# Optimization experiments

Measured on AMD Instinct MI355X. Metric: run time of the kernel, lower is better.

## Reference

```python
import jax, jax.numpy as jnp
import numpy as np

D_MODEL = 768
N_HEADS = 12
HEAD_DIM = D_MODEL // N_HEADS
D_FF = 4 * D_MODEL
EPS = 1e-5


def setup_inputs() -> dict:
    key = jax.random.key(0)
    ks = jax.random.split(key, 16)
    s = 0.02
    x = jax.random.normal(ks[0], (2, 2048, D_MODEL), dtype=jnp.float32)
    wq = jax.random.normal(ks[1], (D_MODEL, D_MODEL), dtype=jnp.float32) * s
    bq = jnp.zeros((D_MODEL,), jnp.float32)
    wk = jax.random.normal(ks[2], (D_MODEL, D_MODEL), dtype=jnp.float32) * s
    bk = jnp.zeros((D_MODEL,), jnp.float32)
    wv = jax.random.normal(ks[3], (D_MODEL, D_MODEL), dtype=jnp.float32) * s
    bv = jnp.zeros((D_MODEL,), jnp.float32)
    wo = jax.random.normal(ks[4], (D_MODEL, D_MODEL), dtype=jnp.float32) * s
    bo = jnp.zeros((D_MODEL,), jnp.float32)
    w1 = jax.random.normal(ks[5], (D_MODEL, D_FF), dtype=jnp.float32) * s
    b1 = jnp.zeros((D_FF,), jnp.float32)
    w2 = jax.random.normal(ks[6], (D_FF, D_MODEL), dtype=jnp.float32) * s
    b2 = jnp.zeros((D_MODEL,), jnp.float32)
    ln1_g = jnp.ones((D_MODEL,), jnp.float32)
    ln1_b = jnp.zeros((D_MODEL,), jnp.float32)
    ln2_g = jnp.ones((D_MODEL,), jnp.float32)
    ln2_b = jnp.zeros((D_MODEL,), jnp.float32)
    return dict(x=x, wq=wq, bq=bq, wk=wk, bk=bk, wv=wv, bv=bv, wo=wo, bo=bo,
                w1=w1, b1=b1, w2=w2, b2=b2,
                ln1_g=ln1_g, ln1_b=ln1_b, ln2_g=ln2_g, ln2_b=ln2_b)


def _layernorm(x, g, b):
    mu = jnp.mean(x, axis=-1, keepdims=True)
    var = jnp.mean(jnp.square(x - mu), axis=-1, keepdims=True)
    return (x - mu) * jax.lax.rsqrt(var + EPS) * g + b


def _attention(x, wq, bq, wk, bk, wv, bv, wo, bo):
    B, S, D = x.shape
    def split_heads(t):  # [B,S,D] -> [B,H,S,Hd]
        return t.reshape(B, S, N_HEADS, HEAD_DIM).transpose(0, 2, 1, 3)
    q = split_heads(x @ wq + bq)
    k = split_heads(x @ wk + bk)
    v = split_heads(x @ wv + bv)
    scores = jnp.einsum('bhqd,bhkd->bhqk', q, k) / np.sqrt(HEAD_DIM).astype(np.float32)
    causal = jnp.tril(jnp.ones((S, S), dtype=bool))
    scores = jnp.where(causal, scores, -jnp.inf)
    weights = jax.nn.softmax(scores, axis=-1)
    attn = jnp.einsum('bhqk,bhkd->bhqd', weights, v)
    attn = attn.transpose(0, 2, 1, 3).reshape(B, S, D)
    return attn @ wo + bo


def reference(x, wq, bq, wk, bk, wv, bv, wo, bo, w1, b1, w2, b2,
              ln1_g, ln1_b, ln2_g, ln2_b):
    x = x + _attention(_layernorm(x, ln1_g, ln1_b), wq, bq, wk, bk, wv, bv, wo, bo)
    h = _layernorm(x, ln2_g, ln2_b)
    ff = jax.nn.relu(h @ w1 + b1) @ w2 + b2
    return x + ff
```

## Files before the change

kernel.cpp:

```cpp
#include <hip/hip_runtime.h>
#include <stdint.h>

typedef __bf16 bf16;
typedef float f32x4 __attribute__((ext_vector_type(4)));
typedef bf16 bf16x8 __attribute__((ext_vector_type(8)));
typedef bf16 bf16x4 __attribute__((ext_vector_type(4)));

#define MFMA16(a, b, c) __builtin_amdgcn_mfma_f32_16x16x32_bf16((a), (b), (c), 0, 0, 0)

static __device__ __forceinline__ void load_lds16(const bf16* g, bf16* l) {
  __builtin_amdgcn_global_load_lds(
      (const __attribute__((address_space(1))) void*)g,
      (__attribute__((address_space(3))) void*)l, 16, 0, 0);
}

__global__ void __launch_bounds__(256) k_transpose(
    const float* s0, const float* s1, const float* s2, const float* s3,
    const float* s4, const float* s5,
    bf16* d0, bf16* d1, bf16* d2, bf16* d3, bf16* d4, bf16* d5) {
  int z = blockIdx.z;
  const float* src; bf16* dst; int R, C;
  switch (z) {
    case 0: src = s0; dst = d0; R = 768;  C = 768;  break;
    case 1: src = s1; dst = d1; R = 768;  C = 768;  break;
    case 2: src = s2; dst = d2; R = 768;  C = 768;  break;
    case 3: src = s3; dst = d3; R = 768;  C = 768;  break;
    case 4: src = s4; dst = d4; R = 768;  C = 3072; break;
    default: src = s5; dst = d5; R = 3072; C = 768; break;
  }
  int tcn = C >> 5;
  int nt = (R >> 5) * tcn;
  int t = blockIdx.x;
  if (t >= nt) return;
  int tr = t / tcn, tc = t % tcn;
  __shared__ float tile[32][33];
  int tx = threadIdx.x & 31, ty = threadIdx.x >> 5;
  for (int i = 0; i < 4; i++)
    tile[ty + i * 8][tx] = src[(size_t)(tr * 32 + ty + i * 8) * C + tc * 32 + tx];
  __syncthreads();
  for (int i = 0; i < 4; i++)
    dst[(size_t)(tc * 32 + ty + i * 8) * R + tr * 32 + tx] = (bf16)tile[tx][ty + i * 8];
}

__global__ void __launch_bounds__(256) k_layernorm(
    const float* __restrict__ in, const float* __restrict__ gam,
    const float* __restrict__ bet, bf16* __restrict__ out) {
  int row = blockIdx.x, tid = threadIdx.x;
  const float* rp = in + (size_t)row * 768;
  float v0 = rp[tid], v1 = rp[tid + 256], v2 = rp[tid + 512];
  float s = v0 + v1 + v2, sq = v0 * v0 + v1 * v1 + v2 * v2;
  for (int off = 1; off < 64; off <<= 1) {
    s += __shfl_xor(s, off, 64);
    sq += __shfl_xor(sq, off, 64);
  }
  __shared__ float ps[8];
  if ((tid & 63) == 0) { ps[tid >> 6] = s; ps[4 + (tid >> 6)] = sq; }
  __syncthreads();
  s = ps[0] + ps[1] + ps[2] + ps[3];
  sq = ps[4] + ps[5] + ps[6] + ps[7];
  float mu = s * (1.0f / 768.0f);
  float rstd = rsqrtf(sq * (1.0f / 768.0f) - mu * mu + 1e-5f);
  bf16* op = out + (size_t)row * 768;
  op[tid] = (bf16)((v0 - mu) * rstd * gam[tid] + bet[tid]);
  op[tid + 256] = (bf16)((v1 - mu) * rstd * gam[tid + 256] + bet[tid + 256]);
  op[tid + 512] = (bf16)((v2 - mu) * rstd * gam[tid + 512] + bet[tid + 512]);
}

__global__ void __launch_bounds__(256) k_ln2_reduce(
    const float* __restrict__ p0, const float* __restrict__ p1,
    const float* __restrict__ x, const float* __restrict__ bo,
    const float* __restrict__ gam, const float* __restrict__ bet,
    float* __restrict__ x1, bf16* __restrict__ h2) {
  int row = blockIdx.x, tid = threadIdx.x;
  size_t base = (size_t)row * 768;
  float v0 = p0[base + tid] + p1[base + tid] + x[base + tid] + bo[tid];
  float v1 = p0[base + tid + 256] + p1[base + tid + 256] + x[base + tid + 256] + bo[tid + 256];
  float v2 = p0[base + tid + 512] + p1[base + tid + 512] + x[base + tid + 512] + bo[tid + 512];
  x1[base + tid] = v0; x1[base + tid + 256] = v1; x1[base + tid + 512] = v2;
  float s = v0 + v1 + v2, sq = v0 * v0 + v1 * v1 + v2 * v2;
  for (int off = 1; off < 64; off <<= 1) {
    s += __shfl_xor(s, off, 64);
    sq += __shfl_xor(sq, off, 64);
  }
  __shared__ float ps[8];
  if ((tid & 63) == 0) { ps[tid >> 6] = s; ps[4 + (tid >> 6)] = sq; }
  __syncthreads();
  s = ps[0] + ps[1] + ps[2] + ps[3];
  sq = ps[4] + ps[5] + ps[6] + ps[7];
  float mu = s * (1.0f / 768.0f);
  float rstd = rsqrtf(sq * (1.0f / 768.0f) - mu * mu + 1e-5f);
  bf16* op = h2 + base;
  op[tid] = (bf16)((v0 - mu) * rstd * gam[tid] + bet[tid]);
  op[tid + 256] = (bf16)((v1 - mu) * rstd * gam[tid + 256] + bet[tid + 256]);
  op[tid + 512] = (bf16)((v2 - mu) * rstd * gam[tid + 512] + bet[tid + 512]);
}

__global__ void __launch_bounds__(256) k_ff2_reduce(
    const float* __restrict__ f0, const float* __restrict__ f1,
    const float* __restrict__ f2, const float* __restrict__ f3,
    const float* __restrict__ x1, const float* __restrict__ b2,
    float* __restrict__ out) {
  size_t i = ((size_t)blockIdx.x * 256 + threadIdx.x) * 4;
  int col = (int)(i % 768);
  f32x4 v = *(const f32x4*)(x1 + i);
  f32x4 b = *(const f32x4*)(b2 + col);
  f32x4 a0 = *(const f32x4*)(f0 + i), a1 = *(const f32x4*)(f1 + i);
  f32x4 a2 = *(const f32x4*)(f2 + i), a3 = *(const f32x4*)(f3 + i);
  *(f32x4*)(out + i) = v + b + a0 + a1 + a2 + a3;
}

template <int MT>
static __device__ __forceinline__ void gemm_core(
    const bf16* __restrict__ A, int lda, const bf16* __restrict__ Bt, int ldb,
    int Kc, int m0, int n0, bf16* As, bf16* Bs, f32x4 acc[MT][4]) {
  int tid = threadIdx.x, w = tid >> 6, lane = tid & 63, quad = lane >> 4, l15 = lane & 15;
  int wr = w >> 1, wc = w & 1;
  int srow = lane >> 2, sk = (lane & 3) * 8;
  const int ABUF = MT * 32 * 32;
  const int BBUF = 128 * 32;

  auto stage = [&](int k0, int buf) {
    bf16* Ab = As + buf * ABUF;
    bf16* Bb = Bs + buf * BBUF;
    if (MT == 4) {
      for (int c = 0; c < 2; c++) {
        int seg = w * 2 + c;
        load_lds16(A + (size_t)(m0 + seg * 16 + srow) * lda + k0 + sk, Ab + seg * 512);
      }
    } else {
      load_lds16(A + (size_t)(m0 + w * 16 + srow) * lda + k0 + sk, Ab + w * 512);
    }
    for (int c = 0; c < 2; c++) {
      int seg = w * 2 + c;
      load_lds16(Bt + (size_t)(n0 + seg * 16 + srow) * ldb + k0 + sk, Bb + seg * 512);
    }
  };

  stage(0, 0);
  int cur = 0;
  for (int k0 = 0; k0 < Kc; k0 += 32) {
    __syncthreads();
    if (k0 + 32 < Kc) stage(k0 + 32, cur ^ 1);
    const bf16* Ab = As + cur * ABUF;
    const bf16* Bb = Bs + cur * BBUF;
    bf16x8 af[MT], bfr[4];
    for (int mi = 0; mi < MT; mi++)
      af[mi] = *(const bf16x8*)(Ab + (wr * (MT * 16) + mi * 16 + l15) * 32 + quad * 8);
    for (int ni = 0; ni < 4; ni++)
      bfr[ni] = *(const bf16x8*)(Bb + (wc * 64 + ni * 16 + l15) * 32 + quad * 8);
    for (int mi = 0; mi < MT; mi++)
      for (int ni = 0; ni < 4; ni++)
        acc[mi][ni] = MFMA16(af[mi], bfr[ni], acc[mi][ni]);
    cur ^= 1;
  }
}

template <int MT>
__global__ void __launch_bounds__(256, 3) k_gemm(
    const bf16* __restrict__ A, const bf16* __restrict__ Bt,
    const float* __restrict__ bias, bf16* __restrict__ outp, int K_, int N_) {
  __shared__ __align__(16) bf16 As[2 * MT * 32 * 32];
  __shared__ __align__(16) bf16 Bs[2 * 128 * 32];
  int m0 = blockIdx.y * (MT * 32), n0 = blockIdx.x * 128;
  f32x4 acc[MT][4] = {};
  gemm_core<MT>(A, K_, Bt, K_, K_, m0, n0, As, Bs, acc);
  int tid = threadIdx.x, w = tid >> 6, lane = tid & 63, quad = lane >> 4, l15 = lane & 15;
  int wr = w >> 1, wc = w & 1;
  float bv[4];
  for (int ni = 0; ni < 4; ni++) bv[ni] = bias[n0 + wc * 64 + ni * 16 + l15];
  for (int mi = 0; mi < MT; mi++) {
    int mb = m0 + wr * (MT * 16) + mi * 16 + quad * 4;
    for (int ni = 0; ni < 4; ni++) {
      int n = n0 + wc * 64 + ni * 16 + l15;
      for (int r = 0; r < 4; r++) {
        float val = acc[mi][ni][r] + bv[ni];
        outp[(size_t)(mb + r) * N_ + n] = (bf16)fmaxf(val, 0.0f);
      }
    }
  }
}

template <int MT>
__global__ void __launch_bounds__(256, 3) k_gemm_split(
    const bf16* __restrict__ A, const bf16* __restrict__ Bt,
    float* __restrict__ f0, float* __restrict__ f1,
    float* __restrict__ f2, float* __restrict__ f3, int K_, int Kc, int N_) {
  __shared__ __align__(16) bf16 As[2 * MT * 32 * 32];
  __shared__ __align__(16) bf16 Bs[2 * 128 * 32];
  int z = blockIdx.z;
  float* outp = (z == 0) ? f0 : (z == 1) ? f1 : (z == 2) ? f2 : f3;
  int m0 = blockIdx.y * (MT * 32), n0 = blockIdx.x * 128;
  f32x4 acc[MT][4] = {};
  gemm_core<MT>(A + (size_t)z * Kc, K_, Bt + (size_t)z * Kc, K_, Kc, m0, n0, As, Bs, acc);
  int tid = threadIdx.x, w = tid >> 6, lane = tid & 63, quad = lane >> 4, l15 = lane & 15;
  int wr = w >> 1, wc = w & 1;
  for (int mi = 0; mi < MT; mi++) {
    int mb = m0 + wr * (MT * 16) + mi * 16 + quad * 4;
    for (int ni = 0; ni < 4; ni++) {
      int n = n0 + wc * 64 + ni * 16 + l15;
      for (int r = 0; r < 4; r++)
        outp[(size_t)(mb + r) * N_ + n] = acc[mi][ni][r];
    }
  }
}

template <int MT>
__global__ void __launch_bounds__(256, 3) k_gemm_qkv(
    const bf16* __restrict__ h1, const bf16* __restrict__ wqT,
    const bf16* __restrict__ wkT, const bf16* __restrict__ wvT,
    const float* __restrict__ bq, const float* __restrict__ bk,
    const float* __restrict__ bv, bf16* __restrict__ qb,
    bf16* __restrict__ kb, bf16* __restrict__ vtb) {
  __shared__ __align__(16) bf16 As[2 * MT * 32 * 32];
  __shared__ __align__(16) bf16 Bs[2 * 128 * 32];
  int z = blockIdx.z;
  const bf16* Bt = (z == 0) ? wqT : (z == 1) ? wkT : wvT;
  const float* bias = (z == 0) ? bq : (z == 1) ? bk : bv;
  int m0 = blockIdx.y * (MT * 32), n0 = blockIdx.x * 128;
  f32x4 acc[MT][4] = {};
  gemm_core<MT>(h1, 768, Bt, 768, 768, m0, n0, As, Bs, acc);
  int tid = threadIdx.x, w = tid >> 6, lane = tid & 63, quad = lane >> 4, l15 = lane & 15;
  int wr = w >> 1, wc = w & 1;
  float bvv[4];
  for (int ni = 0; ni < 4; ni++) bvv[ni] = bias[n0 + wc * 64 + ni * 16 + l15];
  for (int mi = 0; mi < MT; mi++) {
    int mb = m0 + wr * (MT * 16) + mi * 16 + quad * 4;
    int b = mb >> 11, s0_ = mb & 2047;
    for (int ni = 0; ni < 4; ni++) {
      int n = n0 + wc * 64 + ni * 16 + l15;
      int h = n >> 6, hd = n & 63;
      if (z < 2) {
        bf16* outp = (z == 0) ? qb : kb;
        size_t base = (size_t)(b * 12 + h) * 2048 * 64;
        for (int r = 0; r < 4; r++)
          outp[base + (size_t)(s0_ + r) * 64 + hd] = (bf16)(acc[mi][ni][r] + bvv[ni]);
      } else {
        bf16x4 pk;
        for (int r = 0; r < 4; r++) pk[r] = (bf16)(acc[mi][ni][r] + bvv[ni]);
        *(bf16x4*)(vtb + (((size_t)(b * 12 + h) * 64 + hd) * 2048 + s0_)) = pk;
      }
    }
  }
}

__global__ void __launch_bounds__(256, 3) k_attn(
    const bf16* __restrict__ qb, const bf16* __restrict__ kb,
    const bf16* __restrict__ vtb, bf16* __restrict__ out) {
  __shared__ __align__(16) bf16 Ks[2 * 128 * 64];
  __shared__ __align__(16) bf16 Ps[4][16 * 128];
  int qt = 31 - (blockIdx.x / 24);
  int bh = blockIdx.x % 24;
  int q0 = qt * 64;
  int tid = threadIdx.x, w = tid >> 6, lane = tid & 63, quad = lane >> 4, l15 = lane & 15;
  const bf16* qbase = qb + (size_t)bh * 2048 * 64;
  const bf16* kbase = kb + (size_t)bh * 2048 * 64;
  const bf16* vbase = vtb + (size_t)bh * 64 * 2048;

  bf16x8 qf[2];
  for (int ds = 0; ds < 2; ds++)
    qf[ds] = *(const bf16x8*)(qbase + (size_t)(q0 + w * 16 + l15) * 64 + ds * 32 + quad * 8);

  f32x4 o[4] = {};
  f32x4 l_i = {};

  auto stageK = [&](int k0, int buf) {
    int rsub = lane >> 3, c8 = lane & 7;
    bf16* Kb = Ks + buf * (128 * 64);
    for (int c = 0; c < 4; c++) {
      int seg = c * 4 + w;
      int row = seg * 8 + rsub;
      load_lds16(kbase + (size_t)(k0 + row) * 64 + ((c8 ^ (row & 7)) * 8), Kb + seg * 512);
    }
  };

  const float C2 = 0.18033688011112042f;
  int nkt = (qt >> 1) + 1;
  stageK(0, 0);
  int cur = 0;
  for (int kt = 0; kt < nkt; kt++) {
    int k0 = kt * 128;
    __syncthreads();
    if (kt + 1 < nkt) stageK(k0 + 128, cur ^ 1);
    const bf16* Kb = Ks + cur * (128 * 64);

    f32x4 sc[8] = {};
    for (int kj = 0; kj < 8; kj++) {
      int krow = kj * 16 + l15;
      for (int ds = 0; ds < 2; ds++) {
        bf16x8 kf = *(const bf16x8*)(Kb + krow * 64 + (((ds * 4 + quad) ^ (krow & 7)) * 8));
        sc[kj] = MFMA16(qf[ds], kf, sc[kj]);
      }
    }
    if (kt == nkt - 1) {
      int qg = q0 + w * 16 + quad * 4;
      for (int kj = 0; kj < 8; kj++) {
        int kg = k0 + kj * 16 + l15;
        for (int r = 0; r < 4; r++)
          if (kg > qg + r) sc[kj][r] = -3.0e38f;
      }
    }
    f32x4 lsum = {};
    for (int kj = 0; kj < 8; kj++)
      for (int r = 0; r < 4; r++) {
        float p = exp2f(sc[kj][r] * C2);
        sc[kj][r] = p;
        lsum[r] += p;
      }
    for (int off = 1; off < 16; off <<= 1)
      for (int r = 0; r < 4; r++) lsum[r] += __shfl_xor(lsum[r], off, 64);
    for (int r = 0; r < 4; r++) l_i[r] += lsum[r];
    for (int kj = 0; kj < 8; kj++) {
      int colb = kj * 16 + l15;
      int chb = colb >> 3, cin = colb & 7;
      for (int r = 0; r < 4; r++) {
        int prow = quad * 4 + r;
        Ps[w][prow * 128 + ((chb ^ prow) * 8) + cin] = (bf16)sc[kj][r];
      }
    }
    for (int ks = 0; ks < 4; ks++) {
      int prow = l15;
      bf16x8 pf = *(const bf16x8*)(&Ps[w][prow * 128 + (((ks * 4 + quad) ^ prow) * 8)]);
      for (int dj = 0; dj < 4; dj++) {
        int vrow = dj * 16 + l15;
        bf16x8 vf = *(const bf16x8*)(vbase + (size_t)vrow * 2048 + k0 + (ks * 4 + quad) * 8);
        o[dj] = MFMA16(pf, vf, o[dj]);
      }
    }
    cur ^= 1;
  }
  int b = bh / 12, h = bh % 12;
  f32x4 rl;
  for (int r = 0; r < 4; r++) rl[r] = 1.0f / l_i[r];
  int srow = q0 + w * 16 + quad * 4;
  for (int dj = 0; dj < 4; dj++) {
    int d = h * 64 + dj * 16 + l15;
    for (int r = 0; r < 4; r++)
      out[(size_t)(b * 2048 + srow + r) * 768 + d] = (bf16)(o[dj][r] * rl[r]);
  }
}

extern "C" void kernel_launch(void* const* d_in, const int* in_sizes, int n_in,
                              void* d_out, int out_size, void* d_ws, size_t ws_size,
                              hipStream_t stream) {
  const float* x    = (const float*)d_in[0];
  const float* wq   = (const float*)d_in[1];
  const float* bq   = (const float*)d_in[2];
  const float* wk   = (const float*)d_in[3];
  const float* bk   = (const float*)d_in[4];
  const float* wv   = (const float*)d_in[5];
  const float* bv   = (const float*)d_in[6];
  const float* wo   = (const float*)d_in[7];
  const float* bo   = (const float*)d_in[8];
  const float* w1   = (const float*)d_in[9];
  const float* b1   = (const float*)d_in[10];
  const float* w2   = (const float*)d_in[11];
  const float* b2   = (const float*)d_in[12];
  const float* ln1g = (const float*)d_in[13];
  const float* ln1b = (const float*)d_in[14];
  const float* ln2g = (const float*)d_in[15];
  const float* ln2b = (const float*)d_in[16];

  char* p = (char*)d_ws;
  bf16* wqT = (bf16*)p; p += (size_t)768 * 768 * 2;
  bf16* wkT = (bf16*)p; p += (size_t)768 * 768 * 2;
  bf16* wvT = (bf16*)p; p += (size_t)768 * 768 * 2;
  bf16* woT = (bf16*)p; p += (size_t)768 * 768 * 2;
  bf16* w1T = (bf16*)p; p += (size_t)768 * 3072 * 2;
  bf16* w2T = (bf16*)p; p += (size_t)768 * 3072 * 2;
  bf16* h1   = (bf16*)p; p += (size_t)4096 * 768 * 2;
  bf16* qbuf = (bf16*)p; p += (size_t)4096 * 768 * 2;
  bf16* kbuf = (bf16*)p; p += (size_t)4096 * 768 * 2;
  bf16* vtb  = (bf16*)p; p += (size_t)4096 * 768 * 2;
  bf16* att  = (bf16*)p; p += (size_t)4096 * 768 * 2;
  float* x1  = (float*)p; p += (size_t)4096 * 768 * 4;
  bf16* h2   = (bf16*)p; p += (size_t)4096 * 768 * 2;
  bf16* ffm  = (bf16*)p; p += (size_t)4096 * 3072 * 2;
  float* p0  = (float*)p; p += (size_t)4096 * 768 * 4;
  float* p1  = (float*)p; p += (size_t)4096 * 768 * 4;
  float* f0 = (float*)h1;
  float* f1 = (float*)kbuf;
  float* f2 = p0;
  float* f3 = p1;

  k_transpose<<<dim3(2304, 1, 6), dim3(256), 0, stream>>>(
      wq, wk, wv, wo, w1, w2, wqT, wkT, wvT, woT, w1T, w2T);
  k_layernorm<<<dim3(4096), dim3(256), 0, stream>>>(x, ln1g, ln1b, h1);
  k_gemm_qkv<2><<<dim3(6, 64, 3), dim3(256), 0, stream>>>(
      h1, wqT, wkT, wvT, bq, bk, bv, qbuf, kbuf, vtb);
  k_attn<<<dim3(768), dim3(256), 0, stream>>>(qbuf, kbuf, vtb, att);
  k_gemm_split<2><<<dim3(6, 64, 2), dim3(256), 0, stream>>>(
      att, woT, p0, p1, p0, p1, 768, 384, 768);
  k_ln2_reduce<<<dim3(4096), dim3(256), 0, stream>>>(
      p0, p1, x, bo, ln2g, ln2b, x1, h2);
  k_gemm<4><<<dim3(24, 32), dim3(256), 0, stream>>>(
      h2, w1T, b1, ffm, 768, 3072);
  k_gemm_split<4><<<dim3(6, 32, 4), dim3(256), 0, stream>>>(
      ffm, w2T, f0, f1, f2, f3, 3072, 768, 768);
  k_ff2_reduce<<<dim3(3072), dim3(256), 0, stream>>>(
      f0, f1, f2, f3, x1, b2, (float*)d_out);
}
```

Measured before the change: 328.3 us.

## Fuse weight transpose with LN1, stage V tiles in LDS, interleave attention tiles

Merges the weight-transpose and first layernorm kernels into one launch and drops the 6-slice grid that left many blocks idle. In attention, V tiles are now loaded into LDS asynchronously with a swizzled layout instead of read straight from global memory. P is written into the current K buffer after an extra barrier, which frees the separate P array. Query tiles are scheduled alternately from heavy and light causal rows to balance work across blocks. The cost is an extra block-wide sync per key tile and V loads that are not double buffered.

```diff
diff --git a/kernel.cpp b/kernel.cpp
--- a/kernel.cpp
+++ b/kernel.cpp
@@ -14,56 +14,56 @@
       (__attribute__((address_space(3))) void*)l, 16, 0, 0);
 }
 
-__global__ void __launch_bounds__(256) k_transpose(
+__global__ void __launch_bounds__(256) k_prep(
+    const float* __restrict__ x, const float* __restrict__ ln1g,
+    const float* __restrict__ ln1b, bf16* __restrict__ h1,
     const float* s0, const float* s1, const float* s2, const float* s3,
     const float* s4, const float* s5,
     bf16* d0, bf16* d1, bf16* d2, bf16* d3, bf16* d4, bf16* d5) {
-  int z = blockIdx.z;
-  const float* src; bf16* dst; int R, C;
-  switch (z) {
-    case 0: src = s0; dst = d0; R = 768;  C = 768;  break;
-    case 1: src = s1; dst = d1; R = 768;  C = 768;  break;
-    case 2: src = s2; dst = d2; R = 768;  C = 768;  break;
-    case 3: src = s3; dst = d3; R = 768;  C = 768;  break;
-    case 4: src = s4; dst = d4; R = 768;  C = 3072; break;
-    default: src = s5; dst = d5; R = 3072; C = 768; break;
-  }
-  int tcn = C >> 5;
-  int nt = (R >> 5) * tcn;
   int t = blockIdx.x;
-  if (t >= nt) return;
-  int tr = t / tcn, tc = t % tcn;
-  __shared__ float tile[32][33];
-  int tx = threadIdx.x & 31, ty = threadIdx.x >> 5;
-  for (int i = 0; i < 4; i++)
-    tile[ty + i * 8][tx] = src[(size_t)(tr * 32 + ty + i * 8) * C + tc * 32 + tx];
-  __syncthreads();
-  for (int i = 0; i < 4; i++)
-    dst[(size_t)(tc * 32 + ty + i * 8) * R + tr * 32 + tx] = (bf16)tile[tx][ty + i * 8];
-}
-
-__global__ void __launch_bounds__(256) k_layernorm(
-    const float* __restrict__ in, const float* __restrict__ gam,
-    const float* __restrict__ bet, bf16* __restrict__ out) {
-  int row = blockIdx.x, tid = threadIdx.x;
-  const float* rp = in + (size_t)row * 768;
-  float v0 = rp[tid], v1 = rp[tid + 256], v2 = rp[tid + 512];
-  float s = v0 + v1 + v2, sq = v0 * v0 + v1 * v1 + v2 * v2;
-  for (int off = 1; off < 64; off <<= 1) {
-    s += __shfl_xor(s, off, 64);
-    sq += __shfl_xor(sq, off, 64);
-  }
-  __shared__ float ps[8];
-  if ((tid & 63) == 0) { ps[tid >> 6] = s; ps[4 + (tid >> 6)] = sq; }
-  __syncthreads();
-  s = ps[0] + ps[1] + ps[2] + ps[3];
-  sq = ps[4] + ps[5] + ps[6] + ps[7];
-  float mu = s * (1.0f / 768.0f);
-  float rstd = rsqrtf(sq * (1.0f / 768.0f) - mu * mu + 1e-5f);
-  bf16* op = out + (size_t)row * 768;
-  op[tid] = (bf16)((v0 - mu) * rstd * gam[tid] + bet[tid]);
-  op[tid + 256] = (bf16)((v1 - mu) * rstd * gam[tid + 256] + bet[tid + 256]);
-  op[tid + 512] = (bf16)((v2 - mu) * rstd * gam[tid + 512] + bet[tid + 512]);
+  int tid = threadIdx.x;
+  if (t < 6912) {
+    const float* src; bf16* dst; int R, C;
+    if (t < 2304) {
+      int z = t / 576; t -= z * 576;
+      src = (z == 0) ? s0 : (z == 1) ? s1 : (z == 2) ? s2 : s3;
+      dst = (z == 0) ? d0 : (z == 1) ? d1 : (z == 2) ? d2 : d3;
+      R = 768; C = 768;
+    } else if (t < 4608) {
+      t -= 2304; src = s4; dst = d4; R = 768; C = 3072;
+    } else {
+      t -= 4608; src = s5; dst = d5; R = 3072; C = 768;
+    }
+    int tcn = C >> 5;
+    int tr = t / tcn, tc = t % tcn;
+    __shared__ float tile[32][33];
+    int tx = tid & 31, ty = tid >> 5;
+    for (int i = 0; i < 4; i++)
+      tile[ty + i * 8][tx] = src[(size_t)(tr * 32 + ty + i * 8) * C + tc * 32 + tx];
+    __syncthreads();
+    for (int i = 0; i < 4; i++)
+      dst[(size_t)(tc * 32 + ty + i * 8) * R + tr * 32 + tx] = (bf16)tile[tx][ty + i * 8];
+  } else {
+    int row = t - 6912;
+    const float* rp = x + (size_t)row * 768;
+    float v0 = rp[tid], v1 = rp[tid + 256], v2 = rp[tid + 512];
+    float s = v0 + v1 + v2, sq = v0 * v0 + v1 * v1 + v2 * v2;
+    for (int off = 1; off < 64; off <<= 1) {
+      s += __shfl_xor(s, off, 64);
+      sq += __shfl_xor(sq, off, 64);
+    }
+    __shared__ float ps[8];
+    if ((tid & 63) == 0) { ps[tid >> 6] = s; ps[4 + (tid >> 6)] = sq; }
+    __syncthreads();
+    s = ps[0] + ps[1] + ps[2] + ps[3];
+    sq = ps[4] + ps[5] + ps[6] + ps[7];
+    float mu = s * (1.0f / 768.0f);
+    float rstd = rsqrtf(sq * (1.0f / 768.0f) - mu * mu + 1e-5f);
+    bf16* op = h1 + (size_t)row * 768;
+    op[tid] = (bf16)((v0 - mu) * rstd * ln1g[tid] + ln1b[tid]);
+    op[tid + 256] = (bf16)((v1 - mu) * rstd * ln1g[tid + 256] + ln1b[tid + 256]);
+    op[tid + 512] = (bf16)((v2 - mu) * rstd * ln1g[tid + 512] + ln1b[tid + 512]);
+  }
 }
 
 __global__ void __launch_bounds__(256) k_ln2_reduce(
@@ -247,9 +247,10 @@
     const bf16* __restrict__ qb, const bf16* __restrict__ kb,
     const bf16* __restrict__ vtb, bf16* __restrict__ out) {
   __shared__ __align__(16) bf16 Ks[2 * 128 * 64];
-  __shared__ __align__(16) bf16 Ps[4][16 * 128];
-  int qt = 31 - (blockIdx.x / 24);
+  __shared__ __align__(16) bf16 Vs[64 * 128];
+  int g = blockIdx.x / 24;
   int bh = blockIdx.x % 24;
+  int qt = (g & 1) ? (g >> 1) : (31 - (g >> 1));
   int q0 = qt * 64;
   int tid = threadIdx.x, w = tid >> 6, lane = tid & 63, quad = lane >> 4, l15 = lane & 15;
   const bf16* qbase = qb + (size_t)bh * 2048 * 64;
@@ -270,6 +271,14 @@
       int seg = c * 4 + w;
       int row = seg * 8 + rsub;
       load_lds16(kbase + (size_t)(k0 + row) * 64 + ((c8 ^ (row & 7)) * 8), Kb + seg * 512);
+    }
+  };
+  auto stageV = [&](int k0) {
+    int rsub2 = lane >> 4, c16 = lane & 15;
+    for (int c = 0; c < 4; c++) {
+      int seg = c * 4 + w;
+      int row = seg * 4 + rsub2;
+      load_lds16(vbase + (size_t)row * 2048 + k0 + ((c16 ^ (row & 15)) * 8), Vs + seg * 512);
     }
   };
 
@@ -281,7 +290,9 @@
     int k0 = kt * 128;
     __syncthreads();
     if (kt + 1 < nkt) stageK(k0 + 128, cur ^ 1);
+    stageV(k0);
     const bf16* Kb = Ks + cur * (128 * 64);
+    bf16* Pw = Ks + cur * (128 * 64) + w * 2048;
 
     f32x4 sc[8] = {};
     for (int kj = 0; kj < 8; kj++) {
@@ -309,20 +320,23 @@
     for (int off = 1; off < 16; off <<= 1)
       for (int r = 0; r < 4; r++) lsum[r] += __shfl_xor(lsum[r], off, 64);
     for (int r = 0; r < 4; r++) l_i[r] += lsum[r];
+
+    __syncthreads();
+
     for (int kj = 0; kj < 8; kj++) {
       int colb = kj * 16 + l15;
       int chb = colb >> 3, cin = colb & 7;
       for (int r = 0; r < 4; r++) {
         int prow = quad * 4 + r;
-        Ps[w][prow * 128 + ((chb ^ prow) * 8) + cin] = (bf16)sc[kj][r];
+        Pw[prow * 128 + ((chb ^ prow) * 8) + cin] = (bf16)sc[kj][r];
       }
     }
     for (int ks = 0; ks < 4; ks++) {
       int prow = l15;
-      bf16x8 pf = *(const bf16x8*)(&Ps[w][prow * 128 + (((ks * 4 + quad) ^ prow) * 8)]);
+      bf16x8 pf = *(const bf16x8*)(Pw + prow * 128 + (((ks * 4 + quad) ^ prow) * 8));
       for (int dj = 0; dj < 4; dj++) {
         int vrow = dj * 16 + l15;
-        bf16x8 vf = *(const bf16x8*)(vbase + (size_t)vrow * 2048 + k0 + (ks * 4 + quad) * 8);
+        bf16x8 vf = *(const bf16x8*)(Vs + vrow * 128 + (((ks * 4 + quad) ^ (vrow & 15)) * 8));
         o[dj] = MFMA16(pf, vf, o[dj]);
       }
     }
@@ -382,9 +396,8 @@
   float* f2 = p0;
   float* f3 = p1;
 
-  k_transpose<<<dim3(2304, 1, 6), dim3(256), 0, stream>>>(
-      wq, wk, wv, wo, w1, w2, wqT, wkT, wvT, woT, w1T, w2T);
-  k_layernorm<<<dim3(4096), dim3(256), 0, stream>>>(x, ln1g, ln1b, h1);
+  k_prep<<<dim3(11008), dim3(256), 0, stream>>>(
+      x, ln1g, ln1b, h1, wq, wk, wv, wo, w1, w2, wqT, wkT, wvT, woT, w1T, w2T);
   k_gemm_qkv<2><<<dim3(6, 64, 3), dim3(256), 0, stream>>>(
       h1, wqT, wkT, wvT, bq, bk, bv, qbuf, kbuf, vtb);
   k_attn<<<dim3(768), dim3(256), 0, stream>>>(qbuf, kbuf, vtb, att);
```

After: 290.0 us. -11.7%, faster.
